# Optimization experiments

Hardware: AMD Instinct MI355X
Metric: run time of the kernel (lower is better)

## Reference

```python
import jax, jax.numpy as jnp
import numpy as np

A, B, D = 64, 128, 256   # batch, route nodes, feature_dim
H, C = 64, 32            # hidden_capsule, center_num
NUM_ITERS = 3


def _squash(t, axis=-1):
    sq = jnp.sum(t * t, axis=axis, keepdims=True)
    return (sq / (1.0 + sq)) * t / jnp.sqrt(sq)


def _route(priors, n_iters):
    # priors: [K, A, R, D]; dynamic routing over axis=2 (R).
    # Original keeps logits of priors' full shape, but they stay constant
    # along D (init zeros, delta has keepdim on last axis), so [K,A,R,1]
    # is exactly equivalent and avoids a redundant [K,A,R,D] buffer.
    logits = jnp.zeros(priors.shape[:-1] + (1,), priors.dtype)
    outputs = None
    for i in range(n_iters):
        probs = jax.nn.softmax(logits, axis=2)          # [K,A,R,1]
        outputs = _squash(jnp.sum(probs * priors, axis=2, keepdims=True))  # [K,A,1,D]
        if i != n_iters - 1:
            logits = logits + jnp.sum(priors * outputs, axis=-1, keepdims=True)
    return outputs


def setup_inputs() -> dict:
    key = jax.random.key(0)
    k1, k2, k3 = jax.random.split(key, 3)
    x = jax.random.normal(k1, (A, B, D), dtype=jnp.float32)
    route_weights1 = jax.random.normal(k2, (H, D, D), dtype=jnp.float32)
    route_weights = jax.random.normal(k3, (C, D, D), dtype=jnp.float32)
    return {"x": x, "route_weights1": route_weights1, "route_weights": route_weights}


def reference(x, route_weights1, route_weights):
    # stage 1: priors1[h,a,b,:] = x[a,b,:] @ W1[h]  -> [H,A,B,D]
    priors1 = jnp.einsum('abd,hde->habe', x, route_weights1)
    out1 = _route(priors1, NUM_ITERS)                  # [H,A,1,D]
    out1 = jnp.transpose(out1[:, :, 0, :], (1, 0, 2))  # squeeze + transpose(0,1) -> [A,H,D]
    # stage 2: priors[c,a,h,:] = out1[a,h,:] @ W[c]   -> [C,A,H,D]
    priors = jnp.einsum('ahd,cde->cahe', out1, route_weights)
    out = _route(priors, NUM_ITERS)                    # [C,A,1,D]
    return out[:, :, 0, :]                             # squeeze -> [C,A,D]
```

## Files before the change

kernel.cpp:

```cpp
#include <hip/hip_runtime.h>
#include <hip/hip_bf16.h>

typedef __attribute__((ext_vector_type(8))) short bf16x8;
typedef __attribute__((ext_vector_type(4))) float f32x4;
typedef unsigned short u16;
typedef unsigned int u32;

__device__ __forceinline__ u32 bf16_rne(float f) {
  u32 u = __float_as_uint(f);
  return (u + 0x7FFFu + ((u >> 16) & 1u)) >> 16;
}
__device__ __forceinline__ float bf16_val(u32 b) { return __uint_as_float(b << 16); }

__device__ __forceinline__ void g2l16(const u16* g, u16* l) {
  __builtin_amdgcn_global_load_lds(
      (const __attribute__((address_space(1))) u32*)g,
      (__attribute__((address_space(3))) u32*)l, 16, 0, 0);
}

template <int CTRL>
__device__ __forceinline__ float dppmv(float x) {
  return __int_as_float(
      __builtin_amdgcn_mov_dpp(__float_as_int(x), CTRL, 0xF, 0xF, true));
}
__device__ __forceinline__ float rowsum16(float t) {
  t += dppmv<0x128>(t);
  t += dppmv<0x124>(t);
  t += dppmv<0x122>(t);
  t += dppmv<0x121>(t);
  return t;
}
__device__ __forceinline__ float rowmax16(float t) {
  t = fmaxf(t, dppmv<0x128>(t));
  t = fmaxf(t, dppmv<0x124>(t));
  t = fmaxf(t, dppmv<0x122>(t));
  t = fmaxf(t, dppmv<0x121>(t));
  return t;
}

__global__ void split_arr(const float* __restrict__ in,
                          u16* __restrict__ hi, u16* __restrict__ lo, int n4) {
  int i = blockIdx.x * 256 + threadIdx.x;
  if (i >= n4) return;
  float4 v = ((const float4*)in)[i];
  u32 h0 = bf16_rne(v.x), h1 = bf16_rne(v.y), h2 = bf16_rne(v.z), h3 = bf16_rne(v.w);
  u32 l0 = bf16_rne(v.x - bf16_val(h0));
  u32 l1 = bf16_rne(v.y - bf16_val(h1));
  u32 l2 = bf16_rne(v.z - bf16_val(h2));
  u32 l3 = bf16_rne(v.w - bf16_val(h3));
  ushort4 hv; hv.x = (u16)h0; hv.y = (u16)h1; hv.z = (u16)h2; hv.w = (u16)h3;
  ushort4 lv; lv.x = (u16)l0; lv.y = (u16)l1; lv.z = (u16)l2; lv.w = (u16)l3;
  ((ushort4*)hi)[i] = hv;
  ((ushort4*)lo)[i] = lv;
}

__global__ void split_transpose256(const float* __restrict__ in,
                                   u16* __restrict__ hi, u16* __restrict__ lo) {
  __shared__ float tile[32][33];
  const size_t off = (size_t)blockIdx.z * 65536;
  const int tx = threadIdx.x, ty = threadIdx.y;
#pragma unroll
  for (int i = 0; i < 4; ++i) {
    int y = blockIdx.y * 32 + ty + i * 8;
    int x = blockIdx.x * 32 + tx;
    tile[ty + i * 8][tx] = in[off + (size_t)y * 256 + x];
  }
  __syncthreads();
#pragma unroll
  for (int i = 0; i < 4; ++i) {
    float v = tile[tx][ty + i * 8];
    u32 hb = bf16_rne(v);
    u32 lb = bf16_rne(v - bf16_val(hb));
    size_t idx = off + (size_t)(blockIdx.x * 32 + ty + i * 8) * 256 + blockIdx.y * 32 + tx;
    hi[idx] = (u16)hb;
    lo[idx] = (u16)lb;
  }
}

template <int R>
__global__ __launch_bounds__(256, 2) void caps_route(
    const u16* __restrict__ Ahi_g,
    const u16* __restrict__ Alo_g,
    const u16* __restrict__ Whi,
    const u16* __restrict__ Wlo,
    u16* __restrict__ o1hi, u16* __restrict__ o1lo,
    float* __restrict__ outp,
    int KN, int stage) {
  constexpr int APB = 128 / R;
  constexpr int SEG = APB;
  constexpr int MTS = 8 / SEG;
  constexpr int ABS = (R == 128) ? 6 : 5;
  __shared__ __align__(16) u16 Ab[4][8192];
  __shared__ __align__(16) float wlog[2][4][128];
  __shared__ __align__(16) float probs[128];
  __shared__ float sqpart[2][2][4];

  const int tid = threadIdx.x;
  const int w = tid >> 6, lane = tid & 63, q = lane >> 4, li = lane & 15;
  const int eg = w;
  const int kk = blockIdx.x >> ABS;
  const int ab = blockIdx.x & ((1 << ABS) - 1);

  const int sub = lane >> 2, p2 = lane & 3;
  const int gslot = p2 ^ ((sub >> 1) & 3);
  const size_t lane_off = (size_t)sub * 256 + gslot * 8;
  const u16* gAh = Ahi_g + (size_t)ab * 32768 + (size_t)(2 * w) * 4096 + lane_off;
  const u16* gAl = Alo_g + (size_t)ab * 32768 + (size_t)(2 * w) * 4096 + lane_off;

  auto STAGE = [&](int ko, int slot) {
    u16* d = &Ab[slot][(2 * w) * 512] + lane * 8;
    g2l16(gAh + ko, d);
    g2l16(gAh + ko + 4096, d + 512);
    g2l16(gAl + ko, d + 4096);
    g2l16(gAl + ko + 4096, d + 4608);
  };

  const u16* gWh = Whi + (size_t)kk * 65536 + (size_t)(eg * 64 + li) * 256 + q * 8;
  const u16* gWl = Wlo + (size_t)kk * 65536 + (size_t)(eg * 64 + li) * 256 + q * 8;

  const int rslot = q ^ ((li >> 1) & 3);
  const int fbase = li * 32 + rslot * 8;

  f32x4 acc[8][4] = {};

#define MFMA_SLICE(slot)                                                      \
  do {                                                                        \
    const u16* aB = &Ab[slot][0] + fbase;                                     \
    _Pragma("unroll")                                                         \
    for (int mt = 0; mt < 8; ++mt) {                                          \
      bf16x8 ah = *(const bf16x8*)(aB + mt * 512);                            \
      bf16x8 al = *(const bf16x8*)(aB + mt * 512 + 4096);                     \
      _Pragma("unroll")                                                       \
      for (int ct = 0; ct < 4; ++ct) {                                        \
        acc[mt][ct] = __builtin_amdgcn_mfma_f32_16x16x32_bf16(al, bh[ct], acc[mt][ct], 0, 0, 0); \
        acc[mt][ct] = __builtin_amdgcn_mfma_f32_16x16x32_bf16(ah, bl[ct], acc[mt][ct], 0, 0, 0); \
        acc[mt][ct] = __builtin_amdgcn_mfma_f32_16x16x32_bf16(ah, bh[ct], acc[mt][ct], 0, 0, 0); \
      }                                                                       \
    }                                                                         \
  } while (0)

  bf16x8 bh[4], bl[4];
#pragma unroll
  for (int ct = 0; ct < 4; ++ct) {
    bh[ct] = *(const bf16x8*)(gWh + ct * 4096);
    bl[ct] = *(const bf16x8*)(gWl + ct * 4096);
  }
  STAGE(0, 0);
  STAGE(32, 1);
  asm volatile("s_waitcnt vmcnt(0)" ::: "memory");
  __builtin_amdgcn_s_barrier();

#pragma unroll
  for (int p = 0; p < 4; ++p) {
    const int s0 = 2 * p, s1 = 2 * p + 1;
    if (p < 3) {
      STAGE((s0 + 2) * 32, (s0 + 2) & 3);
      STAGE((s1 + 2) * 32, (s1 + 2) & 3);
      __builtin_amdgcn_sched_barrier(0);
    }
    bf16x8 nbh[4], nbl[4];
#pragma unroll
    for (int ct = 0; ct < 4; ++ct) {
      nbh[ct] = *(const bf16x8*)(gWh + ct * 4096 + s1 * 32);
      nbl[ct] = *(const bf16x8*)(gWl + ct * 4096 + s1 * 32);
    }
    MFMA_SLICE(s0 & 3);
#pragma unroll
    for (int ct = 0; ct < 4; ++ct) { bh[ct] = nbh[ct]; bl[ct] = nbl[ct]; }
    if (p < 3) {
#pragma unroll
      for (int ct = 0; ct < 4; ++ct) {
        nbh[ct] = *(const bf16x8*)(gWh + ct * 4096 + (s0 + 2) * 32);
        nbl[ct] = *(const bf16x8*)(gWl + ct * 4096 + (s0 + 2) * 32);
      }
    }
    MFMA_SLICE(s1 & 3);
    if (p < 3) {
#pragma unroll
      for (int ct = 0; ct < 4; ++ct) { bh[ct] = nbh[ct]; bl[ct] = nbl[ct]; }
      asm volatile("s_waitcnt vmcnt(8)" ::: "memory");
      __builtin_amdgcn_s_barrier();
    }
  }
#undef MFMA_SLICE

  const float invR = 1.0f / R;
  float v[SEG][4];
  float scl[SEG];
  float lg0 = 0.f, lg1 = 0.f;

  for (int iter = 0; iter < 3; ++iter) {
    const int par = iter & 1;
    float4 p4[8];
    if (iter == 0) {
#pragma unroll
      for (int mt = 0; mt < 8; ++mt) {
        p4[mt].x = invR; p4[mt].y = invR; p4[mt].z = invR; p4[mt].w = invR;
      }
    } else {
#pragma unroll
      for (int mt = 0; mt < 8; ++mt)
        p4[mt] = *(const float4*)&probs[mt * 16 + q * 4];
    }
    float s[SEG][4];
#pragma unroll
    for (int sg = 0; sg < SEG; ++sg) {
#pragma unroll
      for (int ct = 0; ct < 4; ++ct) {
        float t = 0.f;
#pragma unroll
        for (int mi = 0; mi < MTS; ++mi) {
          const int mt = sg * MTS + mi;
          t += p4[mt].x * acc[mt][ct][0] + p4[mt].y * acc[mt][ct][1] +
               p4[mt].z * acc[mt][ct][2] + p4[mt].w * acc[mt][ct][3];
        }
        t += __shfl_xor(t, 16);
        t += __shfl_xor(t, 32);
        s[sg][ct] = t;
      }
    }
#pragma unroll
    for (int sg = 0; sg < SEG; ++sg) {
      float ss = s[sg][0] * s[sg][0] + s[sg][1] * s[sg][1] +
                 s[sg][2] * s[sg][2] + s[sg][3] * s[sg][3];
      ss = rowsum16(ss);
      if (lane == 0) sqpart[par][sg][eg] = ss;
    }
    if (iter < 2) {
#pragma unroll
      for (int mt = 0; mt < 8; ++mt) {
        const int sg = mt / MTS;
        float tt[4];
#pragma unroll
        for (int rr = 0; rr < 4; ++rr) {
          float t = acc[mt][0][rr] * s[sg][0] + acc[mt][1][rr] * s[sg][1] +
                    acc[mt][2][rr] * s[sg][2] + acc[mt][3][rr] * s[sg][3];
          tt[rr] = rowsum16(t);
        }
        if (li == 0)
          *(float4*)&wlog[par][eg][mt * 16 + q * 4] =
              make_float4(tt[0], tt[1], tt[2], tt[3]);
      }
    }
    __syncthreads();
#pragma unroll
    for (int sg = 0; sg < SEG; ++sg) {
      float sq = sqpart[par][sg][0] + sqpart[par][sg][1] +
                 sqpart[par][sg][2] + sqpart[par][sg][3];
      scl[sg] = (sq > 0.f) ? sq / ((1.0f + sq) * sqrtf(sq)) : 0.f;
#pragma unroll
      for (int ct = 0; ct < 4; ++ct) v[sg][ct] = s[sg][ct] * scl[sg];
    }

    if (iter < 2) {
      int r0 = lane, r1 = lane + 64;
      float d0 = wlog[par][0][r0] + wlog[par][1][r0] + wlog[par][2][r0] + wlog[par][3][r0];
      float d1 = wlog[par][0][r1] + wlog[par][1][r1] + wlog[par][2][r1] + wlog[par][3][r1];
      if (R == 128) {
        lg0 += scl[0] * d0;
        lg1 += scl[0] * d1;
        float m = fmaxf(lg0, lg1);
        m = rowmax16(m);
        m = fmaxf(m, __shfl_xor(m, 16));
        m = fmaxf(m, __shfl_xor(m, 32));
        float e0 = __expf(lg0 - m), e1 = __expf(lg1 - m);
        float zz = e0 + e1;
        zz = rowsum16(zz);
        zz += __shfl_xor(zz, 16);
        zz += __shfl_xor(zz, 32);
        float inv = 1.0f / zz;
        probs[r0] = e0 * inv;
        probs[r1] = e1 * inv;
      } else {
        lg0 += scl[0] * d0;
        lg1 += scl[1] * d1;
        float m0 = rowmax16(lg0), m1 = rowmax16(lg1);
        m0 = fmaxf(m0, __shfl_xor(m0, 16));
        m0 = fmaxf(m0, __shfl_xor(m0, 32));
        m1 = fmaxf(m1, __shfl_xor(m1, 16));
        m1 = fmaxf(m1, __shfl_xor(m1, 32));
        float e0 = __expf(lg0 - m0), e1 = __expf(lg1 - m1);
        float z0 = rowsum16(e0), z1 = rowsum16(e1);
        z0 += __shfl_xor(z0, 16);
        z0 += __shfl_xor(z0, 32);
        z1 += __shfl_xor(z1, 16);
        z1 += __shfl_xor(z1, 32);
        probs[r0] = e0 / z0;
        probs[r1] = e1 / z1;
      }
      asm volatile("s_waitcnt lgkmcnt(0)" ::: "memory");
    }
  }

  if (q == 0) {
#pragma unroll
    for (int sg = 0; sg < SEG; ++sg) {
      const int ag = ab * APB + sg;
      if (stage == 1) {
        size_t ob = ((size_t)ag * KN + kk) * 256;
#pragma unroll
        for (int ct = 0; ct < 4; ++ct) {
          int e = eg * 64 + ct * 16 + li;
          u32 hb = bf16_rne(v[sg][ct]);
          u32 lb = bf16_rne(v[sg][ct] - bf16_val(hb));
          o1hi[ob + e] = (u16)hb;
          o1lo[ob + e] = (u16)lb;
        }
      } else {
        size_t ob = ((size_t)kk * 64 + ag) * 256;
#pragma unroll
        for (int ct = 0; ct < 4; ++ct) {
          int e = eg * 64 + ct * 16 + li;
          outp[ob + e] = v[sg][ct];
        }
      }
    }
  }
}

extern "C" void kernel_launch(void* const* d_in, const int* in_sizes, int n_in,
                              void* d_out, int out_size, void* d_ws, size_t ws_size,
                              hipStream_t stream) {
  const float* x  = (const float*)d_in[0];
  const float* w1 = (const float*)d_in[1];
  const float* wc = (const float*)d_in[2];
  float* out = (float*)d_out;

  char* ws = (char*)d_ws;
  u16* w1hi = (u16*)(ws);
  u16* w1lo = (u16*)(ws + (8u << 20));
  u16* wchi = (u16*)(ws + (16u << 20));
  u16* wclo = (u16*)(ws + (20u << 20));
  u16* xhi  = (u16*)(ws + (24u << 20));
  u16* xlo  = (u16*)(ws + (28u << 20));
  u16* o1hi = (u16*)(ws + (32u << 20));
  u16* o1lo = (u16*)(ws + (34u << 20));

  split_arr<<<2048, 256, 0, stream>>>(x, xhi, xlo, 524288);
  split_transpose256<<<dim3(8, 8, 64), dim3(32, 8), 0, stream>>>(w1, w1hi, w1lo);
  split_transpose256<<<dim3(8, 8, 32), dim3(32, 8), 0, stream>>>(wc, wchi, wclo);
  caps_route<128><<<64 * 64, 256, 0, stream>>>(xhi, xlo, w1hi, w1lo, o1hi, o1lo, nullptr, 64, 1);
  caps_route<64><<<32 * 32, 256, 0, stream>>>(o1hi, o1lo, wchi, wclo, nullptr, nullptr, out, 32, 2);
}
```

Baseline: 335.2 us.

## Switch routing GEMM from 16x16x32 to 32x32x16 MFMA tiles

Replaces the 16x16x32 bf16 MFMA tiling with 32x32x16 MFMA instructions, giving each wave 4x2 tiles of 32x32 accumulators instead of 8x4 tiles of 16x16. The W fragment loads, the LDS A-fragment addressing and the swizzle are reworked for the new operand layout. The post-GEMM routing reductions (weighted sums, squared norms, logit deltas) are rewritten for the 32x32 accumulator lane layout, using 8 partial slots per reduction. The aim is fewer MFMA issues and fewer LDS fragment reads per FLOP. The cost is a changed reduction pattern and extra cross-lane shuffles in the epilogue.

```diff
diff --git a/kernel.cpp b/kernel.cpp
--- a/kernel.cpp
+++ b/kernel.cpp
@@ -2,7 +2,7 @@
 #include <hip/hip_bf16.h>
 
 typedef __attribute__((ext_vector_type(8))) short bf16x8;
-typedef __attribute__((ext_vector_type(4))) float f32x4;
+typedef __attribute__((ext_vector_type(16))) float f32x16;
 typedef unsigned short u16;
 typedef unsigned int u32;
 
@@ -86,17 +86,18 @@
     u16* __restrict__ o1hi, u16* __restrict__ o1lo,
     float* __restrict__ outp,
     int KN, int stage) {
-  constexpr int APB = 128 / R;
-  constexpr int SEG = APB;
-  constexpr int MTS = 8 / SEG;
+  constexpr int SEG = 128 / R;
+  constexpr int MTS = 4 / SEG;
   constexpr int ABS = (R == 128) ? 6 : 5;
   __shared__ __align__(16) u16 Ab[4][8192];
-  __shared__ __align__(16) float wlog[2][4][128];
+  __shared__ __align__(16) float wlog[2][8][128];
   __shared__ __align__(16) float probs[128];
-  __shared__ float sqpart[2][2][4];
+  __shared__ float sqpart[2][2][8];
 
   const int tid = threadIdx.x;
-  const int w = tid >> 6, lane = tid & 63, q = lane >> 4, li = lane & 15;
+  const int w = tid >> 6, lane = tid & 63;
+  const int li = lane & 15, l31 = lane & 31;
+  const int hi = lane >> 5, lh = (lane >> 4) & 1;
   const int eg = w;
   const int kk = blockIdx.x >> ABS;
   const int ab = blockIdx.x & ((1 << ABS) - 1);
@@ -115,36 +116,50 @@
     g2l16(gAl + ko + 4096, d + 4608);
   };
 
-  const u16* gWh = Whi + (size_t)kk * 65536 + (size_t)(eg * 64 + li) * 256 + q * 8;
-  const u16* gWl = Wlo + (size_t)kk * 65536 + (size_t)(eg * 64 + li) * 256 + q * 8;
-
-  const int rslot = q ^ ((li >> 1) & 3);
-  const int fbase = li * 32 + rslot * 8;
-
-  f32x4 acc[8][4] = {};
+  const u16* gWh = Whi + (size_t)kk * 65536 + (size_t)(eg * 64 + l31) * 256 + hi * 8;
+  const u16* gWl = Wlo + (size_t)kk * 65536 + (size_t)(eg * 64 + l31) * 256 + hi * 8;
+
+  const int sw = (li >> 1) & 3;
+  const int aoff0 = lh * 512 + li * 32 + ((hi ^ sw) * 8);
+  const int aoff1 = lh * 512 + li * 32 + (((2 + hi) ^ sw) * 8);
+
+  f32x16 acc[4][2] = {};
+
+#define LOADW(dh, dl, s)                                                \
+  do {                                                                  \
+    _Pragma("unroll")                                                   \
+    for (int ct = 0; ct < 2; ++ct) {                                    \
+      _Pragma("unroll")                                                 \
+      for (int kb = 0; kb < 2; ++kb) {                                  \
+        dh[ct][kb] = *(const bf16x8*)(gWh + ct * 8192 + (s) * 32 + kb * 16); \
+        dl[ct][kb] = *(const bf16x8*)(gWl + ct * 8192 + (s) * 32 + kb * 16); \
+      }                                                                 \
+    }                                                                   \
+  } while (0)
 
 #define MFMA_SLICE(slot)                                                      \
   do {                                                                        \
-    const u16* aB = &Ab[slot][0] + fbase;                                     \
+    const u16* aB = &Ab[slot][0];                                             \
     _Pragma("unroll")                                                         \
-    for (int mt = 0; mt < 8; ++mt) {                                          \
-      bf16x8 ah = *(const bf16x8*)(aB + mt * 512);                            \
-      bf16x8 al = *(const bf16x8*)(aB + mt * 512 + 4096);                     \
+    for (int mt = 0; mt < 4; ++mt) {                                          \
+      bf16x8 ah0 = *(const bf16x8*)(aB + mt * 1024 + aoff0);                  \
+      bf16x8 al0 = *(const bf16x8*)(aB + mt * 1024 + aoff0 + 4096);           \
+      bf16x8 ah1 = *(const bf16x8*)(aB + mt * 1024 + aoff1);                  \
+      bf16x8 al1 = *(const bf16x8*)(aB + mt * 1024 + aoff1 + 4096);           \
       _Pragma("unroll")                                                       \
-      for (int ct = 0; ct < 4; ++ct) {                                        \
-        acc[mt][ct] = __builtin_amdgcn_mfma_f32_16x16x32_bf16(al, bh[ct], acc[mt][ct], 0, 0, 0); \
-        acc[mt][ct] = __builtin_amdgcn_mfma_f32_16x16x32_bf16(ah, bl[ct], acc[mt][ct], 0, 0, 0); \
-        acc[mt][ct] = __builtin_amdgcn_mfma_f32_16x16x32_bf16(ah, bh[ct], acc[mt][ct], 0, 0, 0); \
+      for (int ct = 0; ct < 2; ++ct) {                                        \
+        acc[mt][ct] = __builtin_amdgcn_mfma_f32_32x32x16_bf16(al0, bh[ct][0], acc[mt][ct], 0, 0, 0); \
+        acc[mt][ct] = __builtin_amdgcn_mfma_f32_32x32x16_bf16(ah0, bl[ct][0], acc[mt][ct], 0, 0, 0); \
+        acc[mt][ct] = __builtin_amdgcn_mfma_f32_32x32x16_bf16(ah0, bh[ct][0], acc[mt][ct], 0, 0, 0); \
+        acc[mt][ct] = __builtin_amdgcn_mfma_f32_32x32x16_bf16(al1, bh[ct][1], acc[mt][ct], 0, 0, 0); \
+        acc[mt][ct] = __builtin_amdgcn_mfma_f32_32x32x16_bf16(ah1, bl[ct][1], acc[mt][ct], 0, 0, 0); \
+        acc[mt][ct] = __builtin_amdgcn_mfma_f32_32x32x16_bf16(ah1, bh[ct][1], acc[mt][ct], 0, 0, 0); \
       }                                                                       \
     }                                                                         \
   } while (0)
 
-  bf16x8 bh[4], bl[4];
-#pragma unroll
-  for (int ct = 0; ct < 4; ++ct) {
-    bh[ct] = *(const bf16x8*)(gWh + ct * 4096);
-    bl[ct] = *(const bf16x8*)(gWl + ct * 4096);
-  }
+  bf16x8 bh[2][2], bl[2][2];
+  LOADW(bh, bl, 0);
   STAGE(0, 0);
   STAGE(32, 1);
   asm volatile("s_waitcnt vmcnt(0)" ::: "memory");
@@ -158,104 +173,98 @@
       STAGE((s1 + 2) * 32, (s1 + 2) & 3);
       __builtin_amdgcn_sched_barrier(0);
     }
-    bf16x8 nbh[4], nbl[4];
-#pragma unroll
-    for (int ct = 0; ct < 4; ++ct) {
-      nbh[ct] = *(const bf16x8*)(gWh + ct * 4096 + s1 * 32);
-      nbl[ct] = *(const bf16x8*)(gWl + ct * 4096 + s1 * 32);
-    }
+    bf16x8 nbh[2][2], nbl[2][2];
+    LOADW(nbh, nbl, s1);
     MFMA_SLICE(s0 & 3);
 #pragma unroll
-    for (int ct = 0; ct < 4; ++ct) { bh[ct] = nbh[ct]; bl[ct] = nbl[ct]; }
-    if (p < 3) {
-#pragma unroll
-      for (int ct = 0; ct < 4; ++ct) {
-        nbh[ct] = *(const bf16x8*)(gWh + ct * 4096 + (s0 + 2) * 32);
-        nbl[ct] = *(const bf16x8*)(gWl + ct * 4096 + (s0 + 2) * 32);
-      }
-    }
+    for (int ct = 0; ct < 2; ++ct) {
+#pragma unroll
+      for (int kb = 0; kb < 2; ++kb) { bh[ct][kb] = nbh[ct][kb]; bl[ct][kb] = nbl[ct][kb]; }
+    }
+    if (p < 3) LOADW(nbh, nbl, s0 + 2);
     MFMA_SLICE(s1 & 3);
     if (p < 3) {
 #pragma unroll
-      for (int ct = 0; ct < 4; ++ct) { bh[ct] = nbh[ct]; bl[ct] = nbl[ct]; }
+      for (int ct = 0; ct < 2; ++ct) {
+#pragma unroll
+        for (int kb = 0; kb < 2; ++kb) { bh[ct][kb] = nbh[ct][kb]; bl[ct][kb] = nbl[ct][kb]; }
+      }
       asm volatile("s_waitcnt vmcnt(8)" ::: "memory");
       __builtin_amdgcn_s_barrier();
     }
   }
 #undef MFMA_SLICE
+#undef LOADW
 
   const float invR = 1.0f / R;
-  float v[SEG][4];
+  const int hi4 = hi * 4;
+  float v[SEG][2];
   float scl[SEG];
   float lg0 = 0.f, lg1 = 0.f;
 
   for (int iter = 0; iter < 3; ++iter) {
     const int par = iter & 1;
-    float4 p4[8];
-    if (iter == 0) {
-#pragma unroll
-      for (int mt = 0; mt < 8; ++mt) {
-        p4[mt].x = invR; p4[mt].y = invR; p4[mt].z = invR; p4[mt].w = invR;
-      }
-    } else {
-#pragma unroll
-      for (int mt = 0; mt < 8; ++mt)
-        p4[mt] = *(const float4*)&probs[mt * 16 + q * 4];
-    }
-    float s[SEG][4];
+    float s[SEG][2];
 #pragma unroll
     for (int sg = 0; sg < SEG; ++sg) {
-#pragma unroll
-      for (int ct = 0; ct < 4; ++ct) {
-        float t = 0.f;
-#pragma unroll
-        for (int mi = 0; mi < MTS; ++mi) {
-          const int mt = sg * MTS + mi;
-          t += p4[mt].x * acc[mt][ct][0] + p4[mt].y * acc[mt][ct][1] +
-               p4[mt].z * acc[mt][ct][2] + p4[mt].w * acc[mt][ct][3];
+      float t0 = 0.f, t1 = 0.f;
+#pragma unroll
+      for (int mi = 0; mi < MTS; ++mi) {
+        const int mt = sg * MTS + mi;
+#pragma unroll
+        for (int g = 0; g < 4; ++g) {
+          float4 pv;
+          if (iter == 0) { pv.x = invR; pv.y = invR; pv.z = invR; pv.w = invR; }
+          else           pv = *(const float4*)&probs[mt * 32 + g * 8 + hi4];
+          t0 += pv.x * acc[mt][0][4 * g + 0] + pv.y * acc[mt][0][4 * g + 1] +
+                pv.z * acc[mt][0][4 * g + 2] + pv.w * acc[mt][0][4 * g + 3];
+          t1 += pv.x * acc[mt][1][4 * g + 0] + pv.y * acc[mt][1][4 * g + 1] +
+                pv.z * acc[mt][1][4 * g + 2] + pv.w * acc[mt][1][4 * g + 3];
         }
-        t += __shfl_xor(t, 16);
-        t += __shfl_xor(t, 32);
-        s[sg][ct] = t;
-      }
+      }
+      t0 += __shfl_xor(t0, 32);
+      t1 += __shfl_xor(t1, 32);
+      s[sg][0] = t0; s[sg][1] = t1;
     }
 #pragma unroll
     for (int sg = 0; sg < SEG; ++sg) {
-      float ss = s[sg][0] * s[sg][0] + s[sg][1] * s[sg][1] +
-                 s[sg][2] * s[sg][2] + s[sg][3] * s[sg][3];
+      float ss = s[sg][0] * s[sg][0] + s[sg][1] * s[sg][1];
       ss = rowsum16(ss);
-      if (lane == 0) sqpart[par][sg][eg] = ss;
+      if (li == 0 && hi == 0) sqpart[par][sg][eg * 2 + lh] = ss;
     }
     if (iter < 2) {
 #pragma unroll
-      for (int mt = 0; mt < 8; ++mt) {
+      for (int mt = 0; mt < 4; ++mt) {
         const int sg = mt / MTS;
-        float tt[4];
-#pragma unroll
-        for (int rr = 0; rr < 4; ++rr) {
-          float t = acc[mt][0][rr] * s[sg][0] + acc[mt][1][rr] * s[sg][1] +
-                    acc[mt][2][rr] * s[sg][2] + acc[mt][3][rr] * s[sg][3];
-          tt[rr] = rowsum16(t);
+#pragma unroll
+        for (int g = 0; g < 4; ++g) {
+          float tt0, tt1, tt2, tt3;
+          { float t = acc[mt][0][4*g+0] * s[sg][0] + acc[mt][1][4*g+0] * s[sg][1]; tt0 = rowsum16(t); }
+          { float t = acc[mt][0][4*g+1] * s[sg][0] + acc[mt][1][4*g+1] * s[sg][1]; tt1 = rowsum16(t); }
+          { float t = acc[mt][0][4*g+2] * s[sg][0] + acc[mt][1][4*g+2] * s[sg][1]; tt2 = rowsum16(t); }
+          { float t = acc[mt][0][4*g+3] * s[sg][0] + acc[mt][1][4*g+3] * s[sg][1]; tt3 = rowsum16(t); }
+          if (li == 0)
+            *(float4*)&wlog[par][eg * 2 + lh][mt * 32 + g * 8 + hi4] =
+                make_float4(tt0, tt1, tt2, tt3);
         }
-        if (li == 0)
-          *(float4*)&wlog[par][eg][mt * 16 + q * 4] =
-              make_float4(tt[0], tt[1], tt[2], tt[3]);
       }
     }
     __syncthreads();
 #pragma unroll
     for (int sg = 0; sg < SEG; ++sg) {
-      float sq = sqpart[par][sg][0] + sqpart[par][sg][1] +
-                 sqpart[par][sg][2] + sqpart[par][sg][3];
+      float sq = 0.f;
+#pragma unroll
+      for (int j = 0; j < 8; ++j) sq += sqpart[par][sg][j];
       scl[sg] = (sq > 0.f) ? sq / ((1.0f + sq) * sqrtf(sq)) : 0.f;
-#pragma unroll
-      for (int ct = 0; ct < 4; ++ct) v[sg][ct] = s[sg][ct] * scl[sg];
+      v[sg][0] = s[sg][0] * scl[sg];
+      v[sg][1] = s[sg][1] * scl[sg];
     }
 
     if (iter < 2) {
       int r0 = lane, r1 = lane + 64;
-      float d0 = wlog[par][0][r0] + wlog[par][1][r0] + wlog[par][2][r0] + wlog[par][3][r0];
-      float d1 = wlog[par][0][r1] + wlog[par][1][r1] + wlog[par][2][r1] + wlog[par][3][r1];
+      float d0 = 0.f, d1 = 0.f;
+#pragma unroll
+      for (int j = 0; j < 8; ++j) { d0 += wlog[par][j][r0]; d1 += wlog[par][j][r1]; }
       if (R == 128) {
         lg0 += scl[0] * d0;
         lg1 += scl[0] * d1;
@@ -292,15 +301,15 @@
     }
   }
 
-  if (q == 0) {
+  if (hi == 0) {
 #pragma unroll
     for (int sg = 0; sg < SEG; ++sg) {
-      const int ag = ab * APB + sg;
+      const int ag = ab * SEG + sg;
       if (stage == 1) {
         size_t ob = ((size_t)ag * KN + kk) * 256;
 #pragma unroll
-        for (int ct = 0; ct < 4; ++ct) {
-          int e = eg * 64 + ct * 16 + li;
+        for (int ct = 0; ct < 2; ++ct) {
+          int e = eg * 64 + ct * 32 + l31;
           u32 hb = bf16_rne(v[sg][ct]);
           u32 lb = bf16_rne(v[sg][ct] - bf16_val(hb));
           o1hi[ob + e] = (u16)hb;
@@ -309,8 +318,8 @@
       } else {
         size_t ob = ((size_t)kk * 64 + ag) * 256;
 #pragma unroll
-        for (int ct = 0; ct < 4; ++ct) {
-          int e = eg * 64 + ct * 16 + li;
+        for (int ct = 0; ct < 2; ++ct) {
+          int e = eg * 64 + ct * 32 + l31;
           outp[ob + e] = v[sg][ct];
         }
       }
```

Result: slower. 361.3 us (+7.8%).

## Load A operands directly from global into registers instead of LDS staging

Applied to the files above, without the earlier changes.

The A-matrix tiles are no longer staged into shared memory through global_load_lds with a 4-slot ring buffer and barriers. Each wave now loads its A fragments straight from global memory into registers, prefetching the next fragment one MFMA group ahead. This removes the 64KB LDS buffer and the block barriers, which may raise occupancy. The cost is that all four waves now redundantly load the same A data from global memory or cache, with prefetch only one step deep, so load latency may be exposed.

```diff
diff --git a/kernel.cpp b/kernel.cpp
--- a/kernel.cpp
+++ b/kernel.cpp
@@ -11,12 +11,6 @@
   return (u + 0x7FFFu + ((u >> 16) & 1u)) >> 16;
 }
 __device__ __forceinline__ float bf16_val(u32 b) { return __uint_as_float(b << 16); }
-
-__device__ __forceinline__ void g2l16(const u16* g, u16* l) {
-  __builtin_amdgcn_global_load_lds(
-      (const __attribute__((address_space(1))) u32*)g,
-      (__attribute__((address_space(3))) u32*)l, 16, 0, 0);
-}
 
 template <int CTRL>
 __device__ __forceinline__ float dppmv(float x) {
@@ -86,11 +80,9 @@
     u16* __restrict__ o1hi, u16* __restrict__ o1lo,
     float* __restrict__ outp,
     int KN, int stage) {
-  constexpr int APB = 128 / R;
-  constexpr int SEG = APB;
+  constexpr int SEG = 128 / R;
   constexpr int MTS = 8 / SEG;
   constexpr int ABS = (R == 128) ? 6 : 5;
-  __shared__ __align__(16) u16 Ab[4][8192];
   __shared__ __align__(16) float wlog[2][4][128];
   __shared__ __align__(16) float probs[128];
   __shared__ float sqpart[2][2][4];
@@ -101,43 +93,12 @@
   const int kk = blockIdx.x >> ABS;
   const int ab = blockIdx.x & ((1 << ABS) - 1);
 
-  const int sub = lane >> 2, p2 = lane & 3;
-  const int gslot = p2 ^ ((sub >> 1) & 3);
-  const size_t lane_off = (size_t)sub * 256 + gslot * 8;
-  const u16* gAh = Ahi_g + (size_t)ab * 32768 + (size_t)(2 * w) * 4096 + lane_off;
-  const u16* gAl = Alo_g + (size_t)ab * 32768 + (size_t)(2 * w) * 4096 + lane_off;
-
-  auto STAGE = [&](int ko, int slot) {
-    u16* d = &Ab[slot][(2 * w) * 512] + lane * 8;
-    g2l16(gAh + ko, d);
-    g2l16(gAh + ko + 4096, d + 512);
-    g2l16(gAl + ko, d + 4096);
-    g2l16(gAl + ko + 4096, d + 4608);
-  };
-
+  const u16* gA_h = Ahi_g + (size_t)ab * 32768 + (size_t)li * 256 + q * 8;
+  const u16* gA_l = Alo_g + (size_t)ab * 32768 + (size_t)li * 256 + q * 8;
   const u16* gWh = Whi + (size_t)kk * 65536 + (size_t)(eg * 64 + li) * 256 + q * 8;
   const u16* gWl = Wlo + (size_t)kk * 65536 + (size_t)(eg * 64 + li) * 256 + q * 8;
 
-  const int rslot = q ^ ((li >> 1) & 3);
-  const int fbase = li * 32 + rslot * 8;
-
   f32x4 acc[8][4] = {};
-
-#define MFMA_SLICE(slot)                                                      \
-  do {                                                                        \
-    const u16* aB = &Ab[slot][0] + fbase;                                     \
-    _Pragma("unroll")                                                         \
-    for (int mt = 0; mt < 8; ++mt) {                                          \
-      bf16x8 ah = *(const bf16x8*)(aB + mt * 512);                            \
-      bf16x8 al = *(const bf16x8*)(aB + mt * 512 + 4096);                     \
-      _Pragma("unroll")                                                       \
-      for (int ct = 0; ct < 4; ++ct) {                                        \
-        acc[mt][ct] = __builtin_amdgcn_mfma_f32_16x16x32_bf16(al, bh[ct], acc[mt][ct], 0, 0, 0); \
-        acc[mt][ct] = __builtin_amdgcn_mfma_f32_16x16x32_bf16(ah, bl[ct], acc[mt][ct], 0, 0, 0); \
-        acc[mt][ct] = __builtin_amdgcn_mfma_f32_16x16x32_bf16(ah, bh[ct], acc[mt][ct], 0, 0, 0); \
-      }                                                                       \
-    }                                                                         \
-  } while (0)
 
   bf16x8 bh[4], bl[4];
 #pragma unroll
@@ -145,44 +106,41 @@
     bh[ct] = *(const bf16x8*)(gWh + ct * 4096);
     bl[ct] = *(const bf16x8*)(gWl + ct * 4096);
   }
-  STAGE(0, 0);
-  STAGE(32, 1);
-  asm volatile("s_waitcnt vmcnt(0)" ::: "memory");
-  __builtin_amdgcn_s_barrier();
-
-#pragma unroll
-  for (int p = 0; p < 4; ++p) {
-    const int s0 = 2 * p, s1 = 2 * p + 1;
-    if (p < 3) {
-      STAGE((s0 + 2) * 32, (s0 + 2) & 3);
-      STAGE((s1 + 2) * 32, (s1 + 2) & 3);
-      __builtin_amdgcn_sched_barrier(0);
-    }
+  bf16x8 ahc = *(const bf16x8*)(gA_h);
+  bf16x8 alc = *(const bf16x8*)(gA_l);
+
+#pragma unroll
+  for (int ks = 0; ks < 8; ++ks) {
     bf16x8 nbh[4], nbl[4];
-#pragma unroll
-    for (int ct = 0; ct < 4; ++ct) {
-      nbh[ct] = *(const bf16x8*)(gWh + ct * 4096 + s1 * 32);
-      nbl[ct] = *(const bf16x8*)(gWl + ct * 4096 + s1 * 32);
-    }
-    MFMA_SLICE(s0 & 3);
-#pragma unroll
-    for (int ct = 0; ct < 4; ++ct) { bh[ct] = nbh[ct]; bl[ct] = nbl[ct]; }
-    if (p < 3) {
+    if (ks < 7) {
 #pragma unroll
       for (int ct = 0; ct < 4; ++ct) {
-        nbh[ct] = *(const bf16x8*)(gWh + ct * 4096 + (s0 + 2) * 32);
-        nbl[ct] = *(const bf16x8*)(gWl + ct * 4096 + (s0 + 2) * 32);
-      }
-    }
-    MFMA_SLICE(s1 & 3);
-    if (p < 3) {
+        nbh[ct] = *(const bf16x8*)(gWh + ct * 4096 + (ks + 1) * 32);
+        nbl[ct] = *(const bf16x8*)(gWl + ct * 4096 + (ks + 1) * 32);
+      }
+    }
+#pragma unroll
+    for (int mt = 0; mt < 8; ++mt) {
+      bf16x8 ahn, aln;
+      if (!(mt == 7 && ks == 7)) {
+        const int nmt = (mt + 1) & 7;
+        const int nks = (mt < 7) ? ks : ks + 1;
+        ahn = *(const bf16x8*)(gA_h + nmt * 4096 + nks * 32);
+        aln = *(const bf16x8*)(gA_l + nmt * 4096 + nks * 32);
+      }
+#pragma unroll
+      for (int ct = 0; ct < 4; ++ct) {
+        acc[mt][ct] = __builtin_amdgcn_mfma_f32_16x16x32_bf16(alc, bh[ct], acc[mt][ct], 0, 0, 0);
+        acc[mt][ct] = __builtin_amdgcn_mfma_f32_16x16x32_bf16(ahc, bl[ct], acc[mt][ct], 0, 0, 0);
+        acc[mt][ct] = __builtin_amdgcn_mfma_f32_16x16x32_bf16(ahc, bh[ct], acc[mt][ct], 0, 0, 0);
+      }
+      if (!(mt == 7 && ks == 7)) { ahc = ahn; alc = aln; }
+    }
+    if (ks < 7) {
 #pragma unroll
       for (int ct = 0; ct < 4; ++ct) { bh[ct] = nbh[ct]; bl[ct] = nbl[ct]; }
-      asm volatile("s_waitcnt vmcnt(8)" ::: "memory");
-      __builtin_amdgcn_s_barrier();
-    }
-  }
-#undef MFMA_SLICE
+    }
+  }
 
   const float invR = 1.0f / R;
   float v[SEG][4];
@@ -295,7 +253,7 @@
   if (q == 0) {
 #pragma unroll
     for (int sg = 0; sg < SEG; ++sg) {
-      const int ag = ab * APB + sg;
+      const int ag = ab * SEG + sg;
       if (stage == 1) {
         size_t ob = ((size_t)ag * KN + kk) * 256;
 #pragma unroll
```

Measured after the change: 558.2 us. 1.67x slower.
